# Optimization experiments

Measured on AMD Instinct MI355X. Metric: run time of the kernel, lower is better.

The kernel has to match this reference:

```python
import jax, jax.numpy as jnp
import numpy as np

B, L, H, E = 8, 4096, 8, 64
MODES = 64
IN_CH = H * E   # 512
OUT_CH = H * E  # 512


def setup_inputs() -> dict:
    key = jax.random.key(0)
    kq, kk, kv, kw1, kw2 = jax.random.split(key, 5)
    scale = 1.0 / (IN_CH * OUT_CH)
    return {
        "q": jax.random.normal(kq, (B, L, H, E), jnp.float32),
        "k": jax.random.normal(kk, (B, L, H, E), jnp.float32),
        "v": jax.random.normal(kv, (B, L, H, E), jnp.float32),
        "weights1": scale * jax.random.uniform(kw1, (H, E, E, MODES), jnp.float32),
        "weights2": scale * jax.random.uniform(kw2, (H, E, E, MODES), jnp.float32),
        # mode_select_method='lowest' -> lowest `modes` frequency bins, sorted
        "index_q": jnp.arange(MODES, dtype=jnp.int32),
        "index_kv": jnp.arange(MODES, dtype=jnp.int32),
    }


def reference(q, k, v, weights1, weights2, index_q, index_kv):
    # q, k: [B, L, H, E] -> [B, H, E, L]
    xq = jnp.transpose(q, (0, 2, 3, 1))
    xk = jnp.transpose(k, (0, 2, 3, 1))

    # rFFT along time, then gather the selected frequency modes
    xq_ft_ = jnp.fft.rfft(xq, axis=-1)[..., index_q]    # [B,H,E,Mq] complex64
    xk_ft_ = jnp.fft.rfft(xk, axis=-1)[..., index_kv]   # [B,H,E,Mk]

    # frequency-domain cross attention (plain complex einsum, NO conjugate)
    xqk_ft = jnp.einsum('bhex,bhey->bhxy', xq_ft_, xk_ft_)
    # 'tanh' activation applied to real and imag parts separately
    xqk_ft = jax.lax.complex(jnp.tanh(xqk_ft.real), jnp.tanh(xqk_ft.imag))

    xqkv_ft = jnp.einsum('bhxy,bhey->bhex', xqk_ft, xk_ft_)
    w = jax.lax.complex(weights1, weights2)              # [H,E,O,Mq]
    xqkvw = jnp.einsum('bhex,heox->bhox', xqkv_ft, w)    # [B,H,O,Mq]

    # scatter selected modes back into the full spectrum, then inverse rFFT
    n_freq = L // 2 + 1
    out_ft = jnp.zeros((B, H, E, n_freq), jnp.complex64).at[..., index_q].set(xqkvw)
    out = jnp.fft.irfft(out_ft / (IN_CH * OUT_CH), n=L, axis=-1)  # [B,H,E,L]
    return out
```

## Files before the change

### kernel.cpp

```cpp
#include <hip/hip_runtime.h>
#include <math.h>


#define Lt 4096
#define Ct 512
#define Mt 64

#define TWA_OFF   0u
#define TWJ_OFF   131072u
#define QFP_OFF   655360u
#define COEF_OFF  9043968u

__global__ __launch_bounds__(256) void init_tw(float* __restrict__ twa) {
  int id = blockIdx.x * 256 + threadIdx.x;
  int t = id >> 6, m = id & 63;
  int idx = (m * t) & 4095;
  float a = (float)idx * (1.0f / 2048.0f);
  float s, c;
  sincospif(a, &s, &c);
  twa[t * 128 + 2 * m]     = c;
  twa[t * 128 + 2 * m + 1] = -s;
}

__global__ __launch_bounds__(256) void init_twj(float* __restrict__ twj) {
  int id = blockIdx.x * 256 + threadIdx.x;
  int j = id >> 12, t = id & 4095;
  int m = j >> 1;
  int idx = (m * t) & 4095;
  float a = (float)idx * (1.0f / 2048.0f);
  float s, c;
  sincospif(a, &s, &c);
  twj[id] = (j & 1) ? s : c;
}

__global__ __launch_bounds__(256, 1) void dft_kernel(const float* __restrict__ q,
                                                     const float* __restrict__ k,
                                                     const float* __restrict__ twa,
                                                     float* __restrict__ qfp) {
  const int id   = blockIdx.x;
  const int b    = id & 7;
  const int src  = (id >> 3) & 1;
  const int cblk = (id >> 4) & 1;
  const int ch   = (id >> 5) & 7;
  const int mg   = (id >> 8) & 7;
  const int c    = cblk * 256 + threadIdx.x;
  const float* __restrict__ x = (src ? k : q) + (size_t)b * (Lt * Ct) + c;

  float acc[16];
#pragma unroll
  for (int j = 0; j < 16; ++j) acc[j] = 0.f;

  const int t0 = ch * 128;
  float n0 = x[(size_t)(t0)        * Ct];
  float n1 = x[(size_t)(t0 + 1024) * Ct];
  float n2 = x[(size_t)(t0 + 2048) * Ct];
  float n3 = x[(size_t)(t0 + 3072) * Ct];

  for (int t = t0; t < t0 + 128; ++t) {
    const float x0 = n0, x1 = n1, x2 = n2, x3 = n3;
    const int tn = (t + 1 < t0 + 128) ? (t + 1) : t0;
    n0 = x[(size_t)(tn)        * Ct];
    n1 = x[(size_t)(tn + 1024) * Ct];
    n2 = x[(size_t)(tn + 2048) * Ct];
    n3 = x[(size_t)(tn + 3072) * Ct];

    const float s02 = x0 + x2, s13 = x1 + x3;
    const float A0v = s02 + s13;
    const float A2v = s02 - s13;
    const float D0v = x0 - x2;
    const float D1v = x1 - x3;

    const float4* __restrict__ tw4 = (const float4*)(twa + t * 128 + mg * 16);
#pragma unroll
    for (int l = 0; l < 2; ++l) {
      const float4 wa = tw4[2 * l + 0];
      const float4 wb = tw4[2 * l + 1];
      acc[8 * l + 0] = fmaf(A0v, wa.x, acc[8 * l + 0]);
      acc[8 * l + 1] = fmaf(A0v, wa.y, acc[8 * l + 1]);
      acc[8 * l + 2] = fmaf(D0v, wa.z, fmaf(D1v, wa.w, acc[8 * l + 2]));
      acc[8 * l + 3] = fmaf(D0v, wa.w, fmaf(-D1v, wa.z, acc[8 * l + 3]));
      acc[8 * l + 4] = fmaf(A2v, wb.x, acc[8 * l + 4]);
      acc[8 * l + 5] = fmaf(A2v, wb.y, acc[8 * l + 5]);
      acc[8 * l + 6] = fmaf(D0v, wb.z, fmaf(-D1v, wb.w, acc[8 * l + 6]));
      acc[8 * l + 7] = fmaf(D0v, wb.w, fmaf(D1v, wb.z, acc[8 * l + 7]));
    }
  }

  const int chs = ch * 2 + src;
  float* __restrict__ outp = qfp + (size_t)(chs * 8 + b) * 65536 + (size_t)c * 2;
#pragma unroll
  for (int lm = 0; lm < 8; ++lm) {
    const int m = mg * 8 + lm;
    *(float2*)(outp + (size_t)m * 1024) = make_float2(acc[2 * lm], acc[2 * lm + 1]);
  }
}

__global__ __launch_bounds__(256) void attn_kernel(const float* __restrict__ qfp,
                                                   const float* __restrict__ w1,
                                                   const float* __restrict__ w2,
                                                   float* __restrict__ coefT) {
  __shared__ float2 KS[4096];
  __shared__ float2 QS[1024];

  const int id = blockIdx.x;
  const int b  = id >> 5;
  const int h  = (id >> 2) & 7;
  const int xq = id & 3;
  const int bh = b * 8 + h;

  const int lane = threadIdx.x & 63;
  const int g    = threadIdx.x >> 6;

#pragma unroll 4
  for (int it = 0; it < 16; ++it) {
    const int y = g + 4 * it;
    float kre = 0.f, kim = 0.f;
#pragma unroll
    for (int ch = 0; ch < 8; ++ch) {
      const float2 vk = *(const float2*)(qfp + (size_t)((ch * 2 + 1) * 8 + b) * 65536 +
                                         (size_t)y * 1024 + (size_t)(h * 64 + lane) * 2);
      kre += vk.x; kim += vk.y;
    }
    KS[y * 64 + (lane ^ (y & 31))] = make_float2(kre, kim);
  }
#pragma unroll
  for (int it = 0; it < 4; ++it) {
    const int xl = g + 4 * it;
    const int m  = xq * 16 + xl;
    float qre = 0.f, qim = 0.f;
#pragma unroll
    for (int ch = 0; ch < 8; ++ch) {
      const float2 vq = *(const float2*)(qfp + (size_t)((ch * 2 + 0) * 8 + b) * 65536 +
                                         (size_t)m * 1024 + (size_t)(h * 64 + lane) * 2);
      qre += vq.x; qim += vq.y;
    }
    QS[xl * 64 + (lane ^ xl)] = make_float2(qre, qim);
  }
  __syncthreads();

  {
    const int y = lane;
    float sr[4], si[4];
#pragma unroll
    for (int i = 0; i < 4; ++i) { sr[i] = 0.f; si[i] = 0.f; }
    for (int e = 0; e < 64; ++e) {
      const float2 kv = KS[y * 64 + (e ^ (y & 31))];
#pragma unroll
      for (int xi = 0; xi < 4; ++xi) {
        const int xl = g * 4 + xi;
        const float2 qv = QS[xl * 64 + (e ^ xl)];
        sr[xi] = fmaf(qv.x, kv.x, fmaf(-qv.y, kv.y, sr[xi]));
        si[xi] = fmaf(qv.x, kv.y, fmaf(qv.y, kv.x, si[xi]));
      }
    }
    __syncthreads();
#pragma unroll
    for (int xi = 0; xi < 4; ++xi) {
      const int xl = g * 4 + xi;
      QS[xl * 64 + (y ^ xl)] = make_float2(tanhf(sr[xi]), tanhf(si[xi]));
    }
  }
  __syncthreads();

  {
    const int e = lane;
    float pr[4], pi[4];
#pragma unroll
    for (int i = 0; i < 4; ++i) { pr[i] = 0.f; pi[i] = 0.f; }
    for (int y = 0; y < 64; ++y) {
      const float2 kv = KS[y * 64 + (e ^ (y & 31))];
#pragma unroll
      for (int xi = 0; xi < 4; ++xi) {
        const int xl = g * 4 + xi;
        const float2 sv = QS[xl * 64 + (y ^ xl)];
        pr[xi] = fmaf(sv.x, kv.x, fmaf(-sv.y, kv.y, pr[xi]));
        pi[xi] = fmaf(sv.x, kv.y, fmaf(sv.y, kv.x, pi[xi]));
      }
    }
    __syncthreads();
#pragma unroll
    for (int xi = 0; xi < 4; ++xi) {
      const int xl = g * 4 + xi;
      KS[xl * 64 + (e ^ xl)] = make_float2(pr[xi], pi[xi]);
    }
  }
  __syncthreads();

  {
    const int xs = (threadIdx.x & 3) * 4;
    const int o  = threadIdx.x >> 2;
    float Or[4], Oi[4];
#pragma unroll
    for (int i = 0; i < 4; ++i) { Or[i] = 0.f; Oi[i] = 0.f; }

    const float* __restrict__ w1p = w1 + ((size_t)(h * 64) * 64 + o) * 64 + xq * 16 + xs;
    const float* __restrict__ w2p = w2 + ((size_t)(h * 64) * 64 + o) * 64 + xq * 16 + xs;

#pragma unroll 2
    for (int e = 0; e < 64; ++e) {
      const float4 a1 = *(const float4*)(w1p + (size_t)e * 4096);
      const float4 a2 = *(const float4*)(w2p + (size_t)e * 4096);
      const float wr[4] = {a1.x, a1.y, a1.z, a1.w};
      const float wi[4] = {a2.x, a2.y, a2.z, a2.w};
#pragma unroll
      for (int j = 0; j < 4; ++j) {
        const int xl = xs + j;
        const float2 pv = KS[xl * 64 + (e ^ xl)];
        Or[j] = fmaf(pv.x, wr[j], fmaf(-pv.y, wi[j], Or[j]));
        Oi[j] = fmaf(pv.x, wi[j], fmaf(pv.y, wr[j], Oi[j]));
      }
    }

#pragma unroll
    for (int j = 0; j < 4; ++j) {
      const int xg = xq * 16 + xs + j;
      const float gs = (xg == 0) ? 0x1p-30f : 0x1p-29f;
      coefT[(size_t)(bh * 128 + 2 * xg) * 64 + o]     =  gs * Or[j];
      coefT[(size_t)(bh * 128 + 2 * xg + 1) * 64 + o] = -gs * Oi[j];
    }
  }
}

__global__ __launch_bounds__(256, 1) void idft_kernel(const float* __restrict__ coefT,
                                                      const float* __restrict__ twj,
                                                      float* __restrict__ out) {
  const int bh = blockIdx.x >> 5;
  const int tc = (blockIdx.x >> 1) & 15;
  const int oh = blockIdx.x & 1;
  const int t  = tc * 256 + threadIdx.x;

  float acc[32];
#pragma unroll
  for (int i = 0; i < 32; ++i) acc[i] = 0.f;

  const float* __restrict__ crow = coefT + (size_t)bh * 8192 + oh * 32;

#pragma unroll 2
  for (int j = 0; j < 128; ++j) {
    const float twv = twj[(size_t)j * 4096 + t];
    const float* __restrict__ cj = crow + (size_t)j * 64;
#pragma unroll
    for (int qd = 0; qd < 8; ++qd) {
      const float4 c4 = *(const float4*)(cj + qd * 4);
      acc[qd * 4 + 0] = fmaf(c4.x, twv, acc[qd * 4 + 0]);
      acc[qd * 4 + 1] = fmaf(c4.y, twv, acc[qd * 4 + 1]);
      acc[qd * 4 + 2] = fmaf(c4.z, twv, acc[qd * 4 + 2]);
      acc[qd * 4 + 3] = fmaf(c4.w, twv, acc[qd * 4 + 3]);
    }
  }

  float* __restrict__ orow = out + (size_t)bh * 262144 + (size_t)(oh * 32) * 4096 + t;
#pragma unroll
  for (int ol = 0; ol < 32; ++ol) {
    orow[(size_t)ol * 4096] = acc[ol];
  }
}

extern "C" void kernel_launch(void* const* d_in, const int* in_sizes, int n_in,
                              void* d_out, int out_size, void* d_ws, size_t ws_size,
                              hipStream_t stream) {
  (void)in_sizes; (void)n_in; (void)out_size; (void)ws_size;
  const float* q  = (const float*)d_in[0];
  const float* k  = (const float*)d_in[1];
  const float* w1 = (const float*)d_in[3];
  const float* w2 = (const float*)d_in[4];
  float* ws   = (float*)d_ws;
  float* outp = (float*)d_out;

  float* twa   = ws + TWA_OFF;
  float* twj   = ws + TWJ_OFF;
  float* qfp   = ws + QFP_OFF;
  float* coefT = ws + COEF_OFF;

  init_tw<<<256, 256, 0, stream>>>(twa);
  init_twj<<<2048, 256, 0, stream>>>(twj);
  dft_kernel<<<2048, 256, 0, stream>>>(q, k, twa, qfp);
  attn_kernel<<<256, 256, 0, stream>>>(qfp, w1, w2, coefT);
  idft_kernel<<<2048, 256, 0, stream>>>(coefT, twj, outp);
}
```

Measured before the change: 366.6 us.

## Split DFT into finer time chunks, add separate partial-sum reduce, halve attn work per block

The DFT kernel now splits time into 16 chunks of 64 samples, and each block covers 16 modes instead of 8. Its partial spectra go to the output buffer, which serves as scratch, and a new reduce kernel sums the 16 partials into a compact spectrum. The attention kernel reads those reduced values directly instead of summing partials itself, and uses 512 blocks with 8 query modes each. This is meant to raise parallelism and cut redundant partial-sum reads in attention, at the cost of an extra kernel launch and more partial-sum traffic.

```diff
diff --git a/kernel.cpp b/kernel.cpp
--- a/kernel.cpp
+++ b/kernel.cpp
@@ -8,7 +8,7 @@
 
 #define TWA_OFF   0u
 #define TWJ_OFF   131072u
-#define QFP_OFF   655360u
+#define QF_OFF    655360u
 #define COEF_OFF  9043968u
 
 __global__ __launch_bounds__(256) void init_tw(float* __restrict__ twa) {
@@ -33,7 +33,7 @@
   twj[id] = (j & 1) ? s : c;
 }
 
-__global__ __launch_bounds__(256, 1) void dft_kernel(const float* __restrict__ q,
+__global__ __launch_bounds__(256, 8) void dft_kernel(const float* __restrict__ q,
                                                      const float* __restrict__ k,
                                                      const float* __restrict__ twa,
                                                      float* __restrict__ qfp) {
@@ -41,24 +41,24 @@
   const int b    = id & 7;
   const int src  = (id >> 3) & 1;
   const int cblk = (id >> 4) & 1;
-  const int ch   = (id >> 5) & 7;
-  const int mg   = (id >> 8) & 7;
+  const int ch   = (id >> 5) & 15;
+  const int mg   = (id >> 9) & 3;
   const int c    = cblk * 256 + threadIdx.x;
   const float* __restrict__ x = (src ? k : q) + (size_t)b * (Lt * Ct) + c;
 
-  float acc[16];
-#pragma unroll
-  for (int j = 0; j < 16; ++j) acc[j] = 0.f;
-
-  const int t0 = ch * 128;
+  float acc[32];
+#pragma unroll
+  for (int j = 0; j < 32; ++j) acc[j] = 0.f;
+
+  const int t0 = ch * 64;
   float n0 = x[(size_t)(t0)        * Ct];
   float n1 = x[(size_t)(t0 + 1024) * Ct];
   float n2 = x[(size_t)(t0 + 2048) * Ct];
   float n3 = x[(size_t)(t0 + 3072) * Ct];
 
-  for (int t = t0; t < t0 + 128; ++t) {
+  for (int t = t0; t < t0 + 64; ++t) {
     const float x0 = n0, x1 = n1, x2 = n2, x3 = n3;
-    const int tn = (t + 1 < t0 + 128) ? (t + 1) : t0;
+    const int tn = (t + 1 < t0 + 64) ? (t + 1) : t0;
     n0 = x[(size_t)(tn)        * Ct];
     n1 = x[(size_t)(tn + 1024) * Ct];
     n2 = x[(size_t)(tn + 2048) * Ct];
@@ -70,9 +70,9 @@
     const float D0v = x0 - x2;
     const float D1v = x1 - x3;
 
-    const float4* __restrict__ tw4 = (const float4*)(twa + t * 128 + mg * 16);
-#pragma unroll
-    for (int l = 0; l < 2; ++l) {
+    const float4* __restrict__ tw4 = (const float4*)(twa + t * 128 + mg * 32);
+#pragma unroll
+    for (int l = 0; l < 4; ++l) {
       const float4 wa = tw4[2 * l + 0];
       const float4 wb = tw4[2 * l + 1];
       acc[8 * l + 0] = fmaf(A0v, wa.x, acc[8 * l + 0]);
@@ -89,23 +89,42 @@
   const int chs = ch * 2 + src;
   float* __restrict__ outp = qfp + (size_t)(chs * 8 + b) * 65536 + (size_t)c * 2;
 #pragma unroll
-  for (int lm = 0; lm < 8; ++lm) {
-    const int m = mg * 8 + lm;
+  for (int lm = 0; lm < 16; ++lm) {
+    const int m = mg * 16 + lm;
     *(float2*)(outp + (size_t)m * 1024) = make_float2(acc[2 * lm], acc[2 * lm + 1]);
   }
 }
 
-__global__ __launch_bounds__(256) void attn_kernel(const float* __restrict__ qfp,
+__global__ __launch_bounds__(256, 8) void reduce_kernel(const float* __restrict__ qfp,
+                                                        float* __restrict__ qf) {
+  const int gid = blockIdx.x * 256 + threadIdx.x;
+  const int src = gid >> 17;
+  const int rem = gid & 131071;
+  const int b   = rem >> 14;
+  const int m   = (rem >> 8) & 63;
+  const int c4  = rem & 255;
+
+  const float4* __restrict__ in = (const float4*)qfp + (size_t)m * 256 + c4;
+  float4 s = make_float4(0.f, 0.f, 0.f, 0.f);
+#pragma unroll
+  for (int ch = 0; ch < 16; ++ch) {
+    const float4 v = in[(size_t)((ch * 2 + src) * 8 + b) * 16384];
+    s.x += v.x; s.y += v.y; s.z += v.z; s.w += v.w;
+  }
+  ((float4*)qf)[(size_t)((src * 8 + b) * 64 + m) * 256 + c4] = s;
+}
+
+__global__ __launch_bounds__(256) void attn_kernel(const float* __restrict__ qf,
                                                    const float* __restrict__ w1,
                                                    const float* __restrict__ w2,
                                                    float* __restrict__ coefT) {
   __shared__ float2 KS[4096];
-  __shared__ float2 QS[1024];
+  __shared__ float2 QS[512];
 
   const int id = blockIdx.x;
-  const int b  = id >> 5;
-  const int h  = (id >> 2) & 7;
-  const int xq = id & 3;
+  const int b  = id >> 6;
+  const int h  = (id >> 3) & 7;
+  const int xq = id & 7;
   const int bh = b * 8 + h;
 
   const int lane = threadIdx.x & 63;
@@ -114,40 +133,30 @@
 #pragma unroll 4
   for (int it = 0; it < 16; ++it) {
     const int y = g + 4 * it;
-    float kre = 0.f, kim = 0.f;
-#pragma unroll
-    for (int ch = 0; ch < 8; ++ch) {
-      const float2 vk = *(const float2*)(qfp + (size_t)((ch * 2 + 1) * 8 + b) * 65536 +
-                                         (size_t)y * 1024 + (size_t)(h * 64 + lane) * 2);
-      kre += vk.x; kim += vk.y;
-    }
-    KS[y * 64 + (lane ^ (y & 31))] = make_float2(kre, kim);
-  }
-#pragma unroll
-  for (int it = 0; it < 4; ++it) {
+    const float2 kv = *(const float2*)(qf + (size_t)(8 + b) * 65536 +
+                                       (size_t)y * 1024 + (size_t)(h * 64 + lane) * 2);
+    KS[y * 64 + (lane ^ (y & 31))] = kv;
+  }
+#pragma unroll
+  for (int it = 0; it < 2; ++it) {
     const int xl = g + 4 * it;
-    const int m  = xq * 16 + xl;
-    float qre = 0.f, qim = 0.f;
-#pragma unroll
-    for (int ch = 0; ch < 8; ++ch) {
-      const float2 vq = *(const float2*)(qfp + (size_t)((ch * 2 + 0) * 8 + b) * 65536 +
-                                         (size_t)m * 1024 + (size_t)(h * 64 + lane) * 2);
-      qre += vq.x; qim += vq.y;
-    }
-    QS[xl * 64 + (lane ^ xl)] = make_float2(qre, qim);
+    const int m  = xq * 8 + xl;
+    const float2 qv = *(const float2*)(qf + (size_t)b * 65536 +
+                                       (size_t)m * 1024 + (size_t)(h * 64 + lane) * 2);
+    QS[xl * 64 + (lane ^ xl)] = qv;
   }
   __syncthreads();
 
   {
     const int y = lane;
-    float sr[4], si[4];
-#pragma unroll
-    for (int i = 0; i < 4; ++i) { sr[i] = 0.f; si[i] = 0.f; }
+    float sr[2], si[2];
+#pragma unroll
+    for (int i = 0; i < 2; ++i) { sr[i] = 0.f; si[i] = 0.f; }
     for (int e = 0; e < 64; ++e) {
       const float2 kv = KS[y * 64 + (e ^ (y & 31))];
 #pragma unroll
-      for (int xi = 0; xi < 4; ++xi) {
-        const int xl = g * 4 + xi;
+      for (int xi = 0; xi < 2; ++xi) {
+        const int xl = g * 2 + xi;
         const float2 qv = QS[xl * 64 + (e ^ xl)];
         sr[xi] = fmaf(qv.x, kv.x, fmaf(-qv.y, kv.y, sr[xi]));
         si[xi] = fmaf(qv.x, kv.y, fmaf(qv.y, kv.x, si[xi]));
@@ -155,8 +164,8 @@
     }
     __syncthreads();
 #pragma unroll
-    for (int xi = 0; xi < 4; ++xi) {
-      const int xl = g * 4 + xi;
+    for (int xi = 0; xi < 2; ++xi) {
+      const int xl = g * 2 + xi;
       QS[xl * 64 + (y ^ xl)] = make_float2(tanhf(sr[xi]), tanhf(si[xi]));
     }
   }
@@ -164,14 +173,14 @@
 
   {
     const int e = lane;
-    float pr[4], pi[4];
-#pragma unroll
-    for (int i = 0; i < 4; ++i) { pr[i] = 0.f; pi[i] = 0.f; }
+    float pr[2], pi[2];
+#pragma unroll
+    for (int i = 0; i < 2; ++i) { pr[i] = 0.f; pi[i] = 0.f; }
     for (int y = 0; y < 64; ++y) {
       const float2 kv = KS[y * 64 + (e ^ (y & 31))];
 #pragma unroll
-      for (int xi = 0; xi < 4; ++xi) {
-        const int xl = g * 4 + xi;
+      for (int xi = 0; xi < 2; ++xi) {
+        const int xl = g * 2 + xi;
         const float2 sv = QS[xl * 64 + (y ^ xl)];
         pr[xi] = fmaf(sv.x, kv.x, fmaf(-sv.y, kv.y, pr[xi]));
         pi[xi] = fmaf(sv.x, kv.y, fmaf(sv.y, kv.x, pi[xi]));
@@ -179,31 +188,31 @@
     }
     __syncthreads();
 #pragma unroll
-    for (int xi = 0; xi < 4; ++xi) {
-      const int xl = g * 4 + xi;
+    for (int xi = 0; xi < 2; ++xi) {
+      const int xl = g * 2 + xi;
       KS[xl * 64 + (e ^ xl)] = make_float2(pr[xi], pi[xi]);
     }
   }
   __syncthreads();
 
   {
-    const int xs = (threadIdx.x & 3) * 4;
+    const int xs = (threadIdx.x & 3) * 2;
     const int o  = threadIdx.x >> 2;
-    float Or[4], Oi[4];
-#pragma unroll
-    for (int i = 0; i < 4; ++i) { Or[i] = 0.f; Oi[i] = 0.f; }
-
-    const float* __restrict__ w1p = w1 + ((size_t)(h * 64) * 64 + o) * 64 + xq * 16 + xs;
-    const float* __restrict__ w2p = w2 + ((size_t)(h * 64) * 64 + o) * 64 + xq * 16 + xs;
-
-#pragma unroll 2
+    float Or[2], Oi[2];
+#pragma unroll
+    for (int i = 0; i < 2; ++i) { Or[i] = 0.f; Oi[i] = 0.f; }
+
+    const float* __restrict__ w1p = w1 + ((size_t)(h * 64) * 64 + o) * 64 + xq * 8 + xs;
+    const float* __restrict__ w2p = w2 + ((size_t)(h * 64) * 64 + o) * 64 + xq * 8 + xs;
+
+#pragma unroll 4
     for (int e = 0; e < 64; ++e) {
-      const float4 a1 = *(const float4*)(w1p + (size_t)e * 4096);
-      const float4 a2 = *(const float4*)(w2p + (size_t)e * 4096);
-      const float wr[4] = {a1.x, a1.y, a1.z, a1.w};
-      const float wi[4] = {a2.x, a2.y, a2.z, a2.w};
-#pragma unroll
-      for (int j = 0; j < 4; ++j) {
+      const float2 a1 = *(const float2*)(w1p + (size_t)e * 4096);
+      const float2 a2 = *(const float2*)(w2p + (size_t)e * 4096);
+      const float wr[2] = {a1.x, a1.y};
+      const float wi[2] = {a2.x, a2.y};
+#pragma unroll
+      for (int j = 0; j < 2; ++j) {
         const int xl = xs + j;
         const float2 pv = KS[xl * 64 + (e ^ xl)];
         Or[j] = fmaf(pv.x, wr[j], fmaf(-pv.y, wi[j], Or[j]));
@@ -212,8 +221,8 @@
     }
 
 #pragma unroll
-    for (int j = 0; j < 4; ++j) {
-      const int xg = xq * 16 + xs + j;
+    for (int j = 0; j < 2; ++j) {
+      const int xg = xq * 8 + xs + j;
       const float gs = (xg == 0) ? 0x1p-30f : 0x1p-29f;
       coefT[(size_t)(bh * 128 + 2 * xg) * 64 + o]     =  gs * Or[j];
       coefT[(size_t)(bh * 128 + 2 * xg + 1) * 64 + o] = -gs * Oi[j];
@@ -269,12 +278,14 @@
 
   float* twa   = ws + TWA_OFF;
   float* twj   = ws + TWJ_OFF;
-  float* qfp   = ws + QFP_OFF;
+  float* qf    = ws + QF_OFF;
   float* coefT = ws + COEF_OFF;
+  float* qfp   = outp;
 
   init_tw<<<256, 256, 0, stream>>>(twa);
   init_twj<<<2048, 256, 0, stream>>>(twj);
   dft_kernel<<<2048, 256, 0, stream>>>(q, k, twa, qfp);
-  attn_kernel<<<256, 256, 0, stream>>>(qfp, w1, w2, coefT);
+  reduce_kernel<<<1024, 256, 0, stream>>>(qfp, qf);
+  attn_kernel<<<512, 256, 0, stream>>>(qf, w1, w2, coefT);
   idft_kernel<<<2048, 256, 0, stream>>>(coefT, twj, outp);
 }
```

Result: slower. 553.7 us (+51.0%).
